# Performance work log

Measured on AMD Instinct MI355X. Metric: run time of the kernel, lower is better.

The kernel has to match this reference:

```python
import jax, jax.numpy as jnp
import numpy as np

G, IN_DIM, OUT_DIM = 100000, 256, 128
B, N = 4096, 8192
ALPHA = 0.2          # LeakyReLU negative slope
NEG_INF = -9e15      # same masking constant as the torch module
EPS = 1e-12          # F.normalize eps


def setup_inputs() -> dict:
    key = jax.random.key(0)
    k1, k2, k3, k4, k5, k6, k7 = jax.random.split(key, 7)
    global_feature = jax.random.normal(k1, (G, IN_DIM), dtype=jnp.float32)
    nodes = jax.random.randint(k2, (B,), 0, G, dtype=jnp.int32)
    unique_nodes = jax.random.randint(k3, (N,), 0, G, dtype=jnp.int32)
    mask = jax.random.randint(k4, (B, N), 0, 2, dtype=jnp.int32)
    # ensure every row has at least one neighbor (original always includes self)
    mask = mask.at[:, 0].set(1)
    # xavier_uniform with gain=1.414
    gain = 1.414
    lim_W = gain * np.sqrt(6.0 / (IN_DIM + OUT_DIM))
    W = jax.random.uniform(k5, (IN_DIM, OUT_DIM), jnp.float32, -lim_W, lim_W)
    lim_a = gain * np.sqrt(6.0 / (2 * OUT_DIM + 1))
    a1 = jax.random.uniform(k6, (OUT_DIM,), jnp.float32, -lim_a, lim_a)
    a2 = jax.random.uniform(k7, (OUT_DIM,), jnp.float32, -lim_a, lim_a)
    return {"global_feature": global_feature, "nodes": nodes,
            "unique_nodes": unique_nodes, "mask": mask,
            "W": W, "a1": a1, "a2": a2}


def reference(global_feature, nodes, unique_nodes, mask, W, a1, a2):
    # project gathered features: [B,F], [N,F]
    h_nodes = global_feature[nodes] @ W
    h_neigh = global_feature[unique_nodes] @ W
    # additive attention scores; equivalent to cat([h_i,h_j]) @ a
    e = h_nodes @ a1[:, None] + (h_neigh @ a2)[None, :]   # [B,N]
    e = jnp.where(e >= 0, e, ALPHA * e)                    # leaky relu
    e = jnp.where(mask > 0, e, NEG_INF)
    attention = jax.nn.softmax(e, axis=1)                  # [B,N]
    out = attention @ h_neigh                              # [B,F]
    norm = jnp.linalg.norm(out, axis=1, keepdims=True)
    out = out / jnp.maximum(norm, EPS)                     # F.normalize p=2
    return out
```

## Files before the change

kernel.cpp:

```cpp
#include <hip/hip_runtime.h>
#include <hip/hip_bf16.h>

#define IN_DIM  256
#define OUT_DIM 128
#define B_ROWS  4096
#define N_COLS  8192
#define ALPHA   0.2f
#define NS      16

typedef unsigned short u16;
typedef unsigned int   u32;
typedef __attribute__((ext_vector_type(8))) short short8;
typedef __attribute__((ext_vector_type(4))) float floatx4;

__device__ __forceinline__ float bf2f(u16 v){ return __uint_as_float(((u32)v) << 16); }
__device__ __forceinline__ float bflo(u32 v){ return __uint_as_float(v << 16); }
__device__ __forceinline__ float bfhi(u32 v){ return __uint_as_float(v & 0xffff0000u); }
__device__ __forceinline__ u16 f2bf(float f){
    u32 u = __float_as_uint(f);
    u += 0x7fffu + ((u >> 16) & 1u);
    return (u16)(u >> 16);
}
__device__ __forceinline__ u32 pack_bf16(float a, float b){
    __hip_bfloat162 h = __float22bfloat162_rn(make_float2(a, b));
    return *reinterpret_cast<u32*>(&h);
}

__device__ __forceinline__ int detect_bf16_wave(const u32* __restrict__ g){
    int lane = threadIdx.x & 63;
    uint4 u = ((const uint4*)g)[lane];
#define CHK(x) ((((x) >> 7) & 0xFF) >= 110 && (((x) >> 7) & 0xFF) <= 140)
    unsigned long long c0 = __ballot(CHK(u.x)), c1 = __ballot(CHK(u.y));
    unsigned long long c2 = __ballot(CHK(u.z)), c3 = __ballot(CHK(u.w));
#undef CHK
    int votes = __popcll(c0) + __popcll(c1) + __popcll(c2) + __popcll(c3);
    return votes >= 128;
}

__global__ __launch_bounds__(128) void k_prep(const void* __restrict__ gf,
                                              const void* __restrict__ W, const void* __restrict__ a1,
                                              const void* __restrict__ a2,
                                              u16* __restrict__ WB, float* __restrict__ Wa1,
                                              float* __restrict__ a2f){
    const int isbf = detect_bf16_wave((const u32*)gf);
    const int c  = threadIdx.x;
    const int kb = blockIdx.x;
    float a1c = isbf ? bf2f(((const u16*)a1)[c]) : ((const float*)a1)[c];
    float w[8]; short8 v;
#pragma unroll
    for (int j = 0; j < 8; j++){
        w[j] = isbf ? bf2f(((const u16*)W)[(kb*8 + j) * OUT_DIM + c])
                    : ((const float*)W)[(kb*8 + j) * OUT_DIM + c];
        v[j] = (short)f2bf(w[j]);
    }
    ((short8*)WB)[kb * OUT_DIM + c] = v;

    __shared__ float red[2][8];
    int lane = c & 63, wv = c >> 6;
#pragma unroll
    for (int j = 0; j < 8; j++){
        float p = w[j] * a1c;
        p += __shfl_xor(p, 1);  p += __shfl_xor(p, 2);  p += __shfl_xor(p, 4);
        p += __shfl_xor(p, 8);  p += __shfl_xor(p, 16); p += __shfl_xor(p, 32);
        if (lane == 0) red[wv][j] = p;
    }
    __syncthreads();
    if (c < 8) Wa1[kb*8 + c] = red[0][c] + red[1][c];
    if (kb == 0) a2f[c] = isbf ? bf2f(((const u16*)a2)[c]) : ((const float*)a2)[c];
}

#define HN_BLKS 512
#define ESN_BLKS 1024
#define ZERO_BLKS 128
__global__ __launch_bounds__(256) void k_mid(const void* __restrict__ gf, const int* __restrict__ uniq,
                                             const int* __restrict__ nodes,
                                             const u16* __restrict__ WB, const float* __restrict__ a2f,
                                             const float* __restrict__ Wa1,
                                             u16* __restrict__ hB, float2* __restrict__ esg2,
                                             float2* __restrict__ esn2, float* __restrict__ oacc){
    const int bid = blockIdx.x;
    const int t   = threadIdx.x;

    if (bid < HN_BLKS){
        const int n0   = bid * 16;
        const int lane = t & 63;
        const int wv   = t >> 6;
        const int q    = lane >> 4;
        const int m    = lane & 15;
        const int isbf = detect_bf16_wave((const u32*)gf);
        const int jb0  = wv * 2;

        const size_t row = (size_t)uniq[n0 + m];
        const short8* wb8 = (const short8*)WB;

        floatx4 acc0 = {0.f,0.f,0.f,0.f};
        floatx4 acc1 = {0.f,0.f,0.f,0.f};

#pragma unroll
        for (int ks = 0; ks < IN_DIM/32; ks++){
            short8 afrag;
            if (isbf){
                afrag = *(const short8*)((const u16*)gf + row * IN_DIM + ks*32 + q*8);
            } else {
                const float* gp = (const float*)gf + row * IN_DIM + ks*32 + q*8;
                float4 f0 = *(const float4*)gp;
                float4 f1 = *(const float4*)(gp + 4);
                afrag[0] = (short)f2bf(f0.x); afrag[1] = (short)f2bf(f0.y);
                afrag[2] = (short)f2bf(f0.z); afrag[3] = (short)f2bf(f0.w);
                afrag[4] = (short)f2bf(f1.x); afrag[5] = (short)f2bf(f1.y);
                afrag[6] = (short)f2bf(f1.z); afrag[7] = (short)f2bf(f1.w);
            }
            const int kb = ks*4 + q;
            short8 b0 = wb8[kb * OUT_DIM + jb0*16 + m];
            short8 b1 = wb8[kb * OUT_DIM + (jb0+1)*16 + m];
            acc0 = __builtin_amdgcn_mfma_f32_16x16x32_bf16(afrag, b0, acc0, 0, 0, 0);
            acc1 = __builtin_amdgcn_mfma_f32_16x16x32_bf16(afrag, b1, acc1, 0, 0, 0);
        }

        {
            uint2 v0, v1;
            v0.x = pack_bf16(acc0[0], acc0[1]);
            v0.y = pack_bf16(acc0[2], acc0[3]);
            v1.x = pack_bf16(acc1[0], acc1[1]);
            v1.y = pack_bf16(acc1[2], acc1[3]);
            u16* base = hB + (size_t)(n0/8 + (q>>1)) * 1024 + (q&1)*4;
            *(uint2*)(base + (jb0*16 + m) * 8)     = v0;
            *(uint2*)(base + ((jb0+1)*16 + m) * 8) = v1;
        }

        __shared__ float sred[4][16];
        float a2c0 = a2f[jb0*16 + m], a2c1 = a2f[(jb0+1)*16 + m];
#pragma unroll
        for (int reg = 0; reg < 4; reg++){
            float pr = acc0[reg]*a2c0 + acc1[reg]*a2c1;
            pr += __shfl_xor(pr, 1); pr += __shfl_xor(pr, 2);
            pr += __shfl_xor(pr, 4); pr += __shfl_xor(pr, 8);
            if (m == 0) sred[wv][q*4 + reg] = pr;
        }
        __syncthreads();
        if (t < 16){
            float s = sred[0][t] + sred[1][t] + sred[2][t] + sred[3][t];
            s = fminf(fmaxf(s, -40.f), 40.f);
            esg2[n0 + t] = make_float2(__expf(s), __expf(ALPHA * s));
        }
    } else if (bid < HN_BLKS + ESN_BLKS){
        const int eb = bid - HN_BLKS;
        int lane = t & 63, wv = t >> 6;
        int b = eb * 4 + wv;
        const int isbf = detect_bf16_wave((const u32*)gf);
        float4 wa = ((const float4*)Wa1)[lane];
        float x0, x1, x2, x3;
        if (isbf){
            uint2 gg = ((const uint2*)((const u16*)gf + (size_t)nodes[b] * IN_DIM))[lane];
            x0 = bflo(gg.x); x1 = bfhi(gg.x); x2 = bflo(gg.y); x3 = bfhi(gg.y);
        } else {
            float4 gg = ((const float4*)((const float*)gf + (size_t)nodes[b] * IN_DIM))[lane];
            x0 = gg.x; x1 = gg.y; x2 = gg.z; x3 = gg.w;
        }
        float s = x0*wa.x + x1*wa.y + x2*wa.z + x3*wa.w;
        s += __shfl_xor(s, 1);  s += __shfl_xor(s, 2);  s += __shfl_xor(s, 4);
        s += __shfl_xor(s, 8);  s += __shfl_xor(s, 16); s += __shfl_xor(s, 32);
        if (lane == 0){
            s = fminf(fmaxf(s, -40.f), 40.f);
            esn2[b] = make_float2(__expf(s), __expf(ALPHA * s));
        }
    } else {
        const int zb = bid - (HN_BLKS + ESN_BLKS);
        float4* dst = (float4*)(oacc + (size_t)zb * (B_ROWS*OUT_DIM/ZERO_BLKS));
        float4 z = {0.f,0.f,0.f,0.f};
#pragma unroll
        for (int i = 0; i < 4; i++)
            dst[t + i*256] = z;
    }
}

template<int MODE>
__global__ __launch_bounds__(512) void k_attn(const int* __restrict__ mask,
                                              const float2* __restrict__ esn2,
                                              const float2* __restrict__ esg2,
                                              const u16* __restrict__ hB,
                                              float* __restrict__ obuf){
    const int bid = blockIdx.x;
    const int ns  = bid & (NS-1);
    const int rg  = bid >> 4;
    const int t = threadIdx.x, lane = t & 63, wv = t >> 6;
    const int q = lane >> 4, m = lane & 15;
    const int rowbase = rg*128 + wv*16;
    const int row = rowbase + m;
    const int n0  = ns * (N_COLS/NS);

    __shared__ float4 seg[256];
    __shared__ u16 shb[16*1024];
    if (t < 256){
        const float4* egsrc = (const float4*)esg2 + (n0 >> 1);
        seg[t] = egsrc[t];
    }

    const float2 en = esn2[row];
    const float enx = en.x, eny = en.y;
    const int* mrow = mask + (size_t)row * N_COLS;
    const short8* hb8 = (const short8*)hB;
    short8* shb8 = (short8*)shb;

    floatx4 acc[8];
#pragma unroll
    for (int jb = 0; jb < 8; jb++){ floatx4 z = {0.f,0.f,0.f,0.f}; acc[jb] = z; }

#pragma unroll
    for (int g = 0; g < 4; g++){
        __syncthreads();
        {
            const short8* src = hb8 + (size_t)((n0 >> 3) + g*16) * 128;
#pragma unroll
            for (int i = 0; i < 4; i++) shb8[t + i*512] = src[t + i*512];
        }
        __syncthreads();

#pragma unroll
        for (int kk = 0; kk < 4; kk++){
            const int ks = g*4 + kk;
            const int nn = n0 + ks*32;
            int4 ma = *(const int4*)(mrow + nn + q*8);
            int4 mb = *(const int4*)(mrow + nn + q*8 + 4);
            const float4* egl = &seg[ks*16 + q*4];
            float4 g0 = egl[0], g1 = egl[1], g2 = egl[2], g3 = egl[3];

            float p[8];
#define PEL(j, mk, gx, gy) { float tt = fmaxf(enx * (gx), eny * (gy)); \
                             p[j] = (mk) ? tt : 0.f; }
            PEL(0, ma.x, g0.x, g0.y) PEL(1, ma.y, g0.z, g0.w)
            PEL(2, ma.z, g1.x, g1.y) PEL(3, ma.w, g1.z, g1.w)
            PEL(4, mb.x, g2.x, g2.y) PEL(5, mb.y, g2.z, g2.w)
            PEL(6, mb.z, g3.x, g3.y) PEL(7, mb.w, g3.z, g3.w)
#undef PEL
            uint4 av;
            av.x = pack_bf16(p[0], p[1]); av.y = pack_bf16(p[2], p[3]);
            av.z = pack_bf16(p[4], p[5]); av.w = pack_bf16(p[6], p[7]);
            short8 af = *reinterpret_cast<short8*>(&av);

            const int kbL = kk*4 + q;
#pragma unroll
            for (int jb = 0; jb < 8; jb++){
                short8 bfr = shb8[kbL * OUT_DIM + jb*16 + m];
                acc[jb] = __builtin_amdgcn_mfma_f32_16x16x32_bf16(af, bfr, acc[jb], 0, 0, 0);
            }
        }
    }

    if (MODE >= 1){
        float* prow = obuf + (size_t)ns * (B_ROWS*OUT_DIM);
#pragma unroll
        for (int jb = 0; jb < 8; jb++)
#pragma unroll
            for (int reg = 0; reg < 4; reg++)
                prow[(size_t)(rowbase + q*4 + reg) * OUT_DIM + jb*16 + m] = acc[jb][reg];
    } else {
#pragma unroll
        for (int jb = 0; jb < 8; jb++)
#pragma unroll
            for (int reg = 0; reg < 4; reg++)
                atomicAdd(&obuf[(size_t)(rowbase + q*4 + reg) * OUT_DIM + jb*16 + m], acc[jb][reg]);
    }
}

template<int USE_PART>
__global__ __launch_bounds__(128) void k_norm(const float* __restrict__ obuf,
                                              const void* __restrict__ gf, void* __restrict__ out){
    const int isbf = detect_bf16_wave((const u32*)gf);
    const int b = blockIdx.x, c = threadIdx.x;
    float v;
    if (USE_PART){
        v = 0.f;
#pragma unroll
        for (int ns = 0; ns < NS; ns++)
            v += obuf[(size_t)ns * (B_ROWS*OUT_DIM) + (size_t)b * OUT_DIM + c];
    } else {
        v = obuf[(size_t)b * OUT_DIM + c];
    }
    float ss = v * v;
    for (int off = 32; off > 0; off >>= 1) ss += __shfl_down(ss, off);
    __shared__ float red[2];
    int lane = c & 63, wv = c >> 6;
    if (lane == 0) red[wv] = ss;
    __syncthreads();
    float tot = red[0] + red[1];
    float scale = 1.f / fmaxf(sqrtf(tot), 1e-12f);
    float o = v * scale;
    if (isbf) ((u16*)out)[(size_t)b * OUT_DIM + c] = f2bf(o);
    else      ((float*)out)[(size_t)b * OUT_DIM + c] = o;
}

extern "C" void kernel_launch(void* const* d_in, const int* in_sizes, int n_in,
                              void* d_out, int out_size, void* d_ws, size_t ws_size,
                              hipStream_t stream){
    const void* gf    = d_in[0];
    const int*  nodes = (const int*)d_in[1];
    const int*  uniq  = (const int*)d_in[2];
    const int*  mask  = (const int*)d_in[3];
    const void* W     = d_in[4];
    const void* a1    = d_in[5];
    const void* a2    = d_in[6];

    char* ws = (char*)d_ws;
    u16*    hB   = (u16*)ws;
    u16*    WB   = (u16*)(ws + (2u<<20));
    float2* esg2 = (float2*)(ws + (2u<<20) + (64u<<10));
    float*  Wa1  = (float*)(ws + (2u<<20) + (128u<<10));
    float*  a2f  = (float*)(ws + (2u<<20) + (129u<<10));
    float2* esn2 = (float2*)(ws + (2u<<20) + (130u<<10));
    float*  oacc = (float*)(ws + (4u<<20));
    float*  pbuf = (float*)(ws + (4u<<20));

    const int use_part = (ws_size >= (40u << 20)) ? 1 : 0;
    const int zero_blks = use_part ? 0 : ZERO_BLKS;

    hipLaunchKernelGGL(k_prep, dim3(32), dim3(128), 0, stream, gf, W, a1, a2, WB, Wa1, a2f);
    hipLaunchKernelGGL(k_mid,  dim3(HN_BLKS + ESN_BLKS + zero_blks), dim3(256), 0, stream,
                       gf, uniq, nodes, WB, a2f, Wa1, hB, esg2, esn2, oacc);
    if (use_part){
        hipLaunchKernelGGL(k_attn<1>, dim3((B_ROWS/128)*NS), dim3(512), 0, stream,
                           mask, esn2, esg2, hB, pbuf);
        hipLaunchKernelGGL(k_norm<1>, dim3(B_ROWS), dim3(128), 0, stream, pbuf, gf, d_out);
    } else {
        hipLaunchKernelGGL(k_attn<0>, dim3((B_ROWS/128)*NS), dim3(512), 0, stream,
                           mask, esn2, esg2, hB, oacc);
        hipLaunchKernelGGL(k_norm<0>, dim3(B_ROWS), dim3(128), 0, stream, oacc, gf, d_out);
    }
}
```

Before: 277.9 us.

## Pre-pack int32 attention mask into bitmask before attention kernel

Adds a mask-packing stage inside the middle kernel that uses wave ballots to turn the int32 mask into a bitmask, one bit per column. A new attention-kernel mode then reads 16 packed words per row instead of streaming int4 mask loads inside the MFMA loop. The aim is to take the large mask stream off the attention kernel's critical path and let it run alongside the projection work. The full mask is still read once, plus a small extra write and read of the bitmask, and the new path only runs when the workspace is at least 44 MB.

```diff
diff --git a/kernel.cpp b/kernel.cpp
--- a/kernel.cpp
+++ b/kernel.cpp
@@ -10,6 +10,7 @@
 
 typedef unsigned short u16;
 typedef unsigned int   u32;
+typedef unsigned long long u64;
 typedef __attribute__((ext_vector_type(8))) short short8;
 typedef __attribute__((ext_vector_type(4))) float floatx4;
 
@@ -69,6 +70,7 @@
     if (kb == 0) a2f[c] = isbf ? bf2f(((const u16*)a2)[c]) : ((const float*)a2)[c];
 }
 
+#define PK_BLKS 512
 #define HN_BLKS 512
 #define ESN_BLKS 1024
 #define ZERO_BLKS 128
@@ -77,9 +79,30 @@
                                              const u16* __restrict__ WB, const float* __restrict__ a2f,
                                              const float* __restrict__ Wa1,
                                              u16* __restrict__ hB, float2* __restrict__ esg2,
-                                             float2* __restrict__ esn2, float* __restrict__ oacc){
-    const int bid = blockIdx.x;
-    const int t   = threadIdx.x;
+                                             float2* __restrict__ esn2, float* __restrict__ oacc,
+                                             const int* __restrict__ mask, u64* __restrict__ pb,
+                                             int pk_blks){
+    const int bid0 = blockIdx.x;
+    const int t    = threadIdx.x;
+
+    if (bid0 < pk_blks){
+        const int wid  = bid0*4 + (t >> 6);
+        const int lane = t & 63;
+        const u32* src = (const u32*)mask;
+        for (int it = 0; it < 64; it++){
+            const size_t base = ((size_t)wid*64 + it) * 256;
+            u32 v0 = src[base + lane];
+            u32 v1 = src[base + 64 + lane];
+            u32 v2 = src[base + 128 + lane];
+            u32 v3 = src[base + 192 + lane];
+            u64 b0 = __ballot(v0 != 0), b1 = __ballot(v1 != 0);
+            u64 b2 = __ballot(v2 != 0), b3 = __ballot(v3 != 0);
+            u64 val = (lane == 0) ? b0 : (lane == 1) ? b1 : (lane == 2) ? b2 : b3;
+            if (lane < 4) pb[(base >> 6) + lane] = val;
+        }
+        return;
+    }
+    const int bid = bid0 - pk_blks;
 
     if (bid < HN_BLKS){
         const int n0   = bid * 16;
@@ -176,6 +199,7 @@
 
 template<int MODE>
 __global__ __launch_bounds__(512) void k_attn(const int* __restrict__ mask,
+                                              const u32* __restrict__ pbm32,
                                               const float2* __restrict__ esn2,
                                               const float2* __restrict__ esg2,
                                               const u16* __restrict__ hB,
@@ -196,6 +220,16 @@
         seg[t] = egsrc[t];
     }
 
+    u32 mbits[16];
+    if (MODE == 2){
+        const uint4* pbr = (const uint4*)(pbm32 + (size_t)row * (N_COLS/32) + ns*16);
+        uint4 B0 = pbr[0], B1 = pbr[1], B2 = pbr[2], B3 = pbr[3];
+        mbits[0]=B0.x;  mbits[1]=B0.y;  mbits[2]=B0.z;  mbits[3]=B0.w;
+        mbits[4]=B1.x;  mbits[5]=B1.y;  mbits[6]=B1.z;  mbits[7]=B1.w;
+        mbits[8]=B2.x;  mbits[9]=B2.y;  mbits[10]=B2.z; mbits[11]=B2.w;
+        mbits[12]=B3.x; mbits[13]=B3.y; mbits[14]=B3.z; mbits[15]=B3.w;
+    }
+
     const float2 en = esn2[row];
     const float enx = en.x, eny = en.y;
     const int* mrow = mask + (size_t)row * N_COLS;
@@ -220,19 +254,31 @@
         for (int kk = 0; kk < 4; kk++){
             const int ks = g*4 + kk;
             const int nn = n0 + ks*32;
-            int4 ma = *(const int4*)(mrow + nn + q*8);
-            int4 mb = *(const int4*)(mrow + nn + q*8 + 4);
             const float4* egl = &seg[ks*16 + q*4];
             float4 g0 = egl[0], g1 = egl[1], g2 = egl[2], g3 = egl[3];
 
             float p[8];
+            if (MODE == 2){
+                const u32 w = mbits[ks];
+                const u32 mbyte = (w >> (q*8)) & 0xffu;
+#define PELB(j, gx, gy) { float tt = fmaxf(enx * (gx), eny * (gy)); \
+                          p[j] = (mbyte & (1u << (j))) ? tt : 0.f; }
+                PELB(0, g0.x, g0.y) PELB(1, g0.z, g0.w)
+                PELB(2, g1.x, g1.y) PELB(3, g1.z, g1.w)
+                PELB(4, g2.x, g2.y) PELB(5, g2.z, g2.w)
+                PELB(6, g3.x, g3.y) PELB(7, g3.z, g3.w)
+#undef PELB
+            } else {
+                int4 ma = *(const int4*)(mrow + nn + q*8);
+                int4 mb = *(const int4*)(mrow + nn + q*8 + 4);
 #define PEL(j, mk, gx, gy) { float tt = fmaxf(enx * (gx), eny * (gy)); \
                              p[j] = (mk) ? tt : 0.f; }
-            PEL(0, ma.x, g0.x, g0.y) PEL(1, ma.y, g0.z, g0.w)
-            PEL(2, ma.z, g1.x, g1.y) PEL(3, ma.w, g1.z, g1.w)
-            PEL(4, mb.x, g2.x, g2.y) PEL(5, mb.y, g2.z, g2.w)
-            PEL(6, mb.z, g3.x, g3.y) PEL(7, mb.w, g3.z, g3.w)
+                PEL(0, ma.x, g0.x, g0.y) PEL(1, ma.y, g0.z, g0.w)
+                PEL(2, ma.z, g1.x, g1.y) PEL(3, ma.w, g1.z, g1.w)
+                PEL(4, mb.x, g2.x, g2.y) PEL(5, mb.y, g2.z, g2.w)
+                PEL(6, mb.z, g3.x, g3.y) PEL(7, mb.w, g3.z, g3.w)
 #undef PEL
+            }
             uint4 av;
             av.x = pack_bf16(p[0], p[1]); av.y = pack_bf16(p[2], p[3]);
             av.z = pack_bf16(p[4], p[5]); av.w = pack_bf16(p[6], p[7]);
@@ -310,20 +356,27 @@
     float2* esn2 = (float2*)(ws + (2u<<20) + (130u<<10));
     float*  oacc = (float*)(ws + (4u<<20));
     float*  pbuf = (float*)(ws + (4u<<20));
+    u64*    pbm  = (u64*)(ws + (36u<<20));
 
     const int use_part = (ws_size >= (40u << 20)) ? 1 : 0;
+    const int use_bits = (ws_size >= (44u << 20)) ? 1 : 0;
     const int zero_blks = use_part ? 0 : ZERO_BLKS;
+    const int pk = use_bits ? PK_BLKS : 0;
 
     hipLaunchKernelGGL(k_prep, dim3(32), dim3(128), 0, stream, gf, W, a1, a2, WB, Wa1, a2f);
-    hipLaunchKernelGGL(k_mid,  dim3(HN_BLKS + ESN_BLKS + zero_blks), dim3(256), 0, stream,
-                       gf, uniq, nodes, WB, a2f, Wa1, hB, esg2, esn2, oacc);
-    if (use_part){
+    hipLaunchKernelGGL(k_mid,  dim3(pk + HN_BLKS + ESN_BLKS + zero_blks), dim3(256), 0, stream,
+                       gf, uniq, nodes, WB, a2f, Wa1, hB, esg2, esn2, oacc, mask, pbm, pk);
+    if (use_bits){
+        hipLaunchKernelGGL(k_attn<2>, dim3((B_ROWS/128)*NS), dim3(512), 0, stream,
+                           mask, (const u32*)pbm, esn2, esg2, hB, pbuf);
+        hipLaunchKernelGGL(k_norm<1>, dim3(B_ROWS), dim3(128), 0, stream, pbuf, gf, d_out);
+    } else if (use_part){
         hipLaunchKernelGGL(k_attn<1>, dim3((B_ROWS/128)*NS), dim3(512), 0, stream,
-                           mask, esn2, esg2, hB, pbuf);
+                           mask, (const u32*)pbm, esn2, esg2, hB, pbuf);
         hipLaunchKernelGGL(k_norm<1>, dim3(B_ROWS), dim3(128), 0, stream, pbuf, gf, d_out);
     } else {
         hipLaunchKernelGGL(k_attn<0>, dim3((B_ROWS/128)*NS), dim3(512), 0, stream,
-                           mask, esn2, esg2, hB, oacc);
+                           mask, (const u32*)pbm, esn2, esg2, hB, oacc);
         hipLaunchKernelGGL(k_norm<0>, dim3(B_ROWS), dim3(128), 0, stream, oacc, gf, d_out);
     }
 }
```

Result: slower. 284.1 us (+2.2%).
